# Performance work log

Measured on AMD Instinct MI355X. Metric: run time of the kernel, lower is better.

The kernel has to match this reference:

```python
import jax, jax.numpy as jnp
import numpy as np

P, G, C = 128, 1024, 512
NUM_IDS = 64
EPS_BN = 1e-5


def setup_inputs() -> dict:
    key = jax.random.key(0)
    ks = jax.random.split(key, 20)
    d = jax.random.normal(ks[0], (P, G, C), dtype=jnp.float32)
    y_p = jax.random.randint(ks[1], (P,), 0, NUM_IDS)
    y_g = jax.random.randint(ks[2], (G,), 0, NUM_IDS)
    s = (2.0 / C) ** 0.5  # kaiming-ish scale
    W1 = jax.random.normal(ks[3], (C, C), dtype=jnp.float32) * s
    b1 = jnp.zeros((C,), jnp.float32)
    g1 = 1.0 + 0.02 * jax.random.normal(ks[4], (C,), dtype=jnp.float32)
    be1 = jnp.zeros((C,), jnp.float32)
    rm1 = 0.1 * jax.random.normal(ks[5], (C,), dtype=jnp.float32)
    rv1 = jax.random.uniform(ks[6], (C,), jnp.float32, 0.5, 1.5)
    W2 = jax.random.normal(ks[7], (C, C), dtype=jnp.float32) * s
    b2 = jnp.zeros((C,), jnp.float32)
    g2 = 1.0 + 0.02 * jax.random.normal(ks[8], (C,), dtype=jnp.float32)
    be2 = jnp.zeros((C,), jnp.float32)
    rm2 = 0.1 * jax.random.normal(ks[9], (C,), dtype=jnp.float32)
    rv2 = jax.random.uniform(ks[10], (C,), jnp.float32, 0.5, 1.5)
    # Fc_ClassBlock.classifier: Dropout(0.75) [eval -> identity] + Linear(512, 2)
    Wc = 0.001 * jax.random.normal(ks[11], (C, 2), dtype=jnp.float32)
    bc = jnp.zeros((2,), jnp.float32)
    return dict(d=d, y_p=y_p, y_g=y_g, W1=W1, b1=b1, g1=g1, be1=be1, rm1=rm1, rv1=rv1,
                W2=W2, b2=b2, g2=g2, be2=be2, rm2=rm2, rv2=rv2, Wc=Wc, bc=bc)


def _bn(x, g, b, m, v):
    return (x - m) * jax.lax.rsqrt(v + EPS_BN) * g + b


def _lrelu(x):
    return jnp.where(x >= 0, x, 0.1 * x)


def _preprocess_adj(w):
    # adj = w + I; symmetric normalization D^-1/2 adj^T D^-1/2 (literal torch order)
    adj = w + jnp.eye(w.shape[0], dtype=w.dtype)
    d_inv_sqrt = jax.lax.rsqrt(adj.sum(axis=1))  # rowsum >= 1 due to self-loops
    return d_inv_sqrt[:, None] * adj.T * d_inv_sqrt[None, :]


def reference(d, y_p, y_g, W1, b1, g1, be1, rm1, rv1, W2, b2, g2, be2, rm2, rv2, Wc, bc):
    # label[i, j] = (y_p[i] == y_g[j])
    label = (y_p[:, None] == y_g[None, :]).astype(jnp.int64)
    # hard_weight adjacency: w[i, j] = (y_g[i] == y_g[j])
    w = (y_g[:, None] == y_g[None, :]).astype(jnp.float32)
    w = _preprocess_adj(w)  # [G, G]
    # ReFineBlock (eval mode: BN running stats, dropout off); BN per-feature so flatten P*G
    h = d.reshape(-1, C)
    h = _lrelu(_bn(h @ W1 + b1, g1, be1, rm1, rv1))
    h = _lrelu(_bn(h @ W2 + b2, g2, be2, rm2, rv2))
    t = h.reshape(P, G, C)
    # per-channel torch.mm(t[:, :, i], w) fused into one batched contraction
    d_new = jnp.einsum('pgc,gh->phc', t, w)
    # classifier.classifier: Linear(512, 2) (dropout eval -> identity)
    result = d_new.reshape(-1, C) @ Wc + bc  # [P*G, 2]
    return result, label.reshape(-1)
```

## Files before the change

kernel.cpp:

```cpp
#include <hip/hip_runtime.h>
#include <hip/hip_bf16.h>

#define P_DIM 128
#define G_DIM 1024
#define C_DIM 512
#define M_DIM (P_DIM * G_DIM)
#define NUM_IDS 64
#define RESULT_ELEMS (M_DIM * 2)
#define LABEL_ELEMS  (M_DIM)

typedef __bf16 bf16;
typedef __bf16 bf16x8 __attribute__((ext_vector_type(8)));
typedef float f32x4 __attribute__((ext_vector_type(4)));

constexpr int BM = 64;
constexpr int BK = 32;
constexpr int BNC = 128;
constexpr int APITCH = 40;
constexpr int BPITCH = 40;
constexpr int HPITCH = 520;

__global__ void prep_kernel(const float* __restrict__ b1, const float* __restrict__ g1,
                            const float* __restrict__ be1, const float* __restrict__ rm1,
                            const float* __restrict__ rv1,
                            const float* __restrict__ b2, const float* __restrict__ g2,
                            const float* __restrict__ be2, const float* __restrict__ rm2,
                            const float* __restrict__ rv2,
                            const int* __restrict__ y_g,
                            float* __restrict__ alpha1, float* __restrict__ beta1,
                            float* __restrict__ alpha2, float* __restrict__ beta2,
                            float* __restrict__ inv)
{
    __shared__ int cnt[NUM_IDS];
    int tid = threadIdx.x;
    if (tid < NUM_IDS) cnt[tid] = 0;
    __syncthreads();
    if (tid < C_DIM) {
        float s1 = g1[tid] * rsqrtf(rv1[tid] + 1e-5f);
        alpha1[tid] = s1;
        beta1[tid]  = (b1[tid] - rm1[tid]) * s1 + be1[tid];
        float s2 = g2[tid] * rsqrtf(rv2[tid] + 1e-5f);
        alpha2[tid] = s2;
        beta2[tid]  = (b2[tid] - rm2[tid]) * s2 + be2[tid];
    }
    for (int h = tid; h < G_DIM; h += 512) atomicAdd(&cnt[y_g[h]], 1);
    __syncthreads();
    if (tid < NUM_IDS) inv[tid] = 1.0f / (float)(cnt[tid] + 1);
}

__global__ __launch_bounds__(256) void transpose_scale(
    const float* __restrict__ W, const float* __restrict__ s, bf16* __restrict__ WT)
{
    __shared__ float tile[64][65];
    const int k0 = blockIdx.x * 64, n0 = blockIdx.y * 64;
    const int t = threadIdx.x;
    const int c = t & 63, r4 = t >> 6;
#pragma unroll
    for (int it = 0; it < 16; ++it) {
        int k = r4 + it * 4;
        tile[k][c] = W[(size_t)(k0 + k) * C_DIM + n0 + c];
    }
    __syncthreads();
#pragma unroll
    for (int it = 0; it < 16; ++it) {
        int n = r4 + it * 4;
        float sv = s[n0 + n];
        WT[(size_t)(n0 + n) * C_DIM + k0 + c] = (bf16)(tile[c][n] * sv);
    }
}

__global__ __launch_bounds__(256, 2) void fused_gnn(
    const float* __restrict__ d,
    const bf16* __restrict__ W1T, const float* __restrict__ beta1,
    const bf16* __restrict__ W2T, const float* __restrict__ beta2,
    const float* __restrict__ Wc, float* __restrict__ u)
{
    __shared__ union {
        bf16  As[BM][APITCH];
        float ur[BM][2];
    } sA;
    __shared__ bf16 Bs[BNC][BPITCH];
    __shared__ bf16 h1s[BM][HPITCH];

    const int tid = threadIdx.x;
    const int ln  = tid & 63;
    const int wid = tid >> 6;
    const int wm  = wid & 1;
    const int wn  = wid >> 1;
    const int l15 = ln & 15;
    const int lg  = ln >> 4;
    const size_t gm0 = (size_t)blockIdx.x * BM;

    const int ar = tid >> 2;
    const int aq = (tid & 3) * 8;
    const int bn = tid >> 1;
    const int bq = (tid & 1) * 16;

    for (int chunk = 0; chunk < 4; ++chunk) {
        const int n0 = chunk * BNC;
        f32x4 acc[2][4];
#pragma unroll
        for (int fm = 0; fm < 2; ++fm)
#pragma unroll
            for (int fn = 0; fn < 4; ++fn)
                acc[fm][fn] = (f32x4){0.f, 0.f, 0.f, 0.f};

        float4 pa0 = *(const float4*)(d + (gm0 + ar) * C_DIM + aq);
        float4 pa1 = *(const float4*)(d + (gm0 + ar) * C_DIM + aq + 4);
        float4 pb0 = *(const float4*)(W1T + (size_t)(n0 + bn) * C_DIM + bq);
        float4 pb1 = *(const float4*)(W1T + (size_t)(n0 + bn) * C_DIM + bq + 8);

        for (int k0 = 0; k0 < C_DIM; k0 += BK) {
            __syncthreads();
            {
                bf16x8 av;
                av[0]=(bf16)pa0.x; av[1]=(bf16)pa0.y; av[2]=(bf16)pa0.z; av[3]=(bf16)pa0.w;
                av[4]=(bf16)pa1.x; av[5]=(bf16)pa1.y; av[6]=(bf16)pa1.z; av[7]=(bf16)pa1.w;
                *(bf16x8*)&sA.As[ar][aq] = av;
                *(float4*)&Bs[bn][bq]     = pb0;
                *(float4*)&Bs[bn][bq + 8] = pb1;
            }
            __syncthreads();
            if (k0 + BK < C_DIM) {
                pa0 = *(const float4*)(d + (gm0 + ar) * C_DIM + (k0 + BK) + aq);
                pa1 = *(const float4*)(d + (gm0 + ar) * C_DIM + (k0 + BK) + aq + 4);
                pb0 = *(const float4*)(W1T + (size_t)(n0 + bn) * C_DIM + (k0 + BK) + bq);
                pb1 = *(const float4*)(W1T + (size_t)(n0 + bn) * C_DIM + (k0 + BK) + bq + 8);
            }
            bf16x8 af[2], bfr[4];
#pragma unroll
            for (int fm = 0; fm < 2; ++fm)
                af[fm] = *(const bf16x8*)&sA.As[wm * 32 + fm * 16 + l15][lg * 8];
#pragma unroll
            for (int fn = 0; fn < 4; ++fn)
                bfr[fn] = *(const bf16x8*)&Bs[wn * 64 + fn * 16 + l15][lg * 8];
#pragma unroll
            for (int fm = 0; fm < 2; ++fm)
#pragma unroll
                for (int fn = 0; fn < 4; ++fn)
                    acc[fm][fn] = __builtin_amdgcn_mfma_f32_16x16x32_bf16(
                        af[fm], bfr[fn], acc[fm][fn], 0, 0, 0);
        }
#pragma unroll
        for (int fn = 0; fn < 4; ++fn) {
            int c = n0 + wn * 64 + fn * 16 + l15;
            float be = beta1[c];
#pragma unroll
            for (int fm = 0; fm < 2; ++fm) {
                int mrow = wm * 32 + fm * 16 + lg * 4;
#pragma unroll
                for (int j = 0; j < 4; ++j) {
                    float v = acc[fm][fn][j] + be;
                    v = v >= 0.f ? v : 0.1f * v;
                    h1s[mrow + j][c] = (bf16)v;
                }
            }
        }
    }

    __syncthreads();
    if (tid < BM * 2) sA.ur[tid >> 1][tid & 1] = 0.f;

    float pu0[2][4] = {}, pu1[2][4] = {};
    for (int chunk = 0; chunk < 4; ++chunk) {
        const int n0 = chunk * BNC;
        f32x4 acc[2][4];
#pragma unroll
        for (int fm = 0; fm < 2; ++fm)
#pragma unroll
            for (int fn = 0; fn < 4; ++fn)
                acc[fm][fn] = (f32x4){0.f, 0.f, 0.f, 0.f};

        float4 pb0 = *(const float4*)(W2T + (size_t)(n0 + bn) * C_DIM + bq);
        float4 pb1 = *(const float4*)(W2T + (size_t)(n0 + bn) * C_DIM + bq + 8);

        for (int k0 = 0; k0 < C_DIM; k0 += BK) {
            __syncthreads();
            *(float4*)&Bs[bn][bq]     = pb0;
            *(float4*)&Bs[bn][bq + 8] = pb1;
            __syncthreads();
            if (k0 + BK < C_DIM) {
                pb0 = *(const float4*)(W2T + (size_t)(n0 + bn) * C_DIM + (k0 + BK) + bq);
                pb1 = *(const float4*)(W2T + (size_t)(n0 + bn) * C_DIM + (k0 + BK) + bq + 8);
            }
            bf16x8 af[2], bfr[4];
#pragma unroll
            for (int fm = 0; fm < 2; ++fm)
                af[fm] = *(const bf16x8*)&h1s[wm * 32 + fm * 16 + l15][k0 + lg * 8];
#pragma unroll
            for (int fn = 0; fn < 4; ++fn)
                bfr[fn] = *(const bf16x8*)&Bs[wn * 64 + fn * 16 + l15][lg * 8];
#pragma unroll
            for (int fm = 0; fm < 2; ++fm)
#pragma unroll
                for (int fn = 0; fn < 4; ++fn)
                    acc[fm][fn] = __builtin_amdgcn_mfma_f32_16x16x32_bf16(
                        af[fm], bfr[fn], acc[fm][fn], 0, 0, 0);
        }
#pragma unroll
        for (int fn = 0; fn < 4; ++fn) {
            int c = n0 + wn * 64 + fn * 16 + l15;
            float be = beta2[c];
            float w0 = Wc[2 * c], w1 = Wc[2 * c + 1];
#pragma unroll
            for (int fm = 0; fm < 2; ++fm)
#pragma unroll
                for (int j = 0; j < 4; ++j) {
                    float v = acc[fm][fn][j] + be;
                    v = v >= 0.f ? v : 0.1f * v;
                    pu0[fm][j] = fmaf(v, w0, pu0[fm][j]);
                    pu1[fm][j] = fmaf(v, w1, pu1[fm][j]);
                }
        }
    }
#pragma unroll
    for (int s = 1; s < 16; s <<= 1)
#pragma unroll
        for (int fm = 0; fm < 2; ++fm)
#pragma unroll
            for (int j = 0; j < 4; ++j) {
                pu0[fm][j] += __shfl_xor(pu0[fm][j], s, 64);
                pu1[fm][j] += __shfl_xor(pu1[fm][j], s, 64);
            }
    if (l15 == 0) {
#pragma unroll
        for (int fm = 0; fm < 2; ++fm)
#pragma unroll
            for (int j = 0; j < 4; ++j) {
                int mrow = wm * 32 + fm * 16 + lg * 4 + j;
                atomicAdd(&sA.ur[mrow][0], pu0[fm][j]);
                atomicAdd(&sA.ur[mrow][1], pu1[fm][j]);
            }
    }
    __syncthreads();
    if (tid < BM * 2) {
        int r = tid >> 1, comp = tid & 1;
        u[(gm0 + r) * 2 + comp] = sA.ur[r][comp];
    }
}

__global__ void finalize_kernel(const float* __restrict__ u, const int* __restrict__ y_g,
                                const float* __restrict__ inv, const float* __restrict__ bc,
                                float* __restrict__ out)
{
    int p = blockIdx.x;
    int tid = threadIdx.x;
    __shared__ float su[NUM_IDS][2];
    if (tid < NUM_IDS * 2) su[tid >> 1][tid & 1] = 0.f;
    __syncthreads();
    for (int h = tid; h < G_DIM; h += 256) {
        int k = y_g[h];
        const float* up = u + ((size_t)p * G_DIM + h) * 2;
        atomicAdd(&su[k][0], up[0]);
        atomicAdd(&su[k][1], up[1]);
    }
    __syncthreads();
    float bc0 = bc[0], bc1 = bc[1];
    for (int h = tid; h < G_DIM; h += 256) {
        int k = y_g[h];
        float iv = inv[k];
        size_t r = (size_t)p * G_DIM + h;
        out[r * 2 + 0] = (su[k][0] + u[r * 2 + 0]) * iv + bc0;
        out[r * 2 + 1] = (su[k][1] + u[r * 2 + 1]) * iv + bc1;
    }
}

__global__ void label_kernel(const int* __restrict__ y_p, const int* __restrict__ y_g,
                             float* __restrict__ outF, long long* __restrict__ outL, int mode)
{
    int i = blockIdx.x * 256 + threadIdx.x;
    if (i >= LABEL_ELEMS) return;
    int p = i >> 10;
    int g = i & 1023;
    long long lab = (y_p[p] == y_g[g]) ? 1 : 0;
    if (mode == 1) outF[i] = (float)lab;
    else           outL[i] = lab;
}

extern "C" void kernel_launch(void* const* d_in, const int* in_sizes, int n_in,
                              void* d_out, int out_size, void* d_ws, size_t ws_size,
                              hipStream_t stream) {
    const float* d   = (const float*)d_in[0];
    const int*   y_p = (const int*)d_in[1];
    const int*   y_g = (const int*)d_in[2];
    const float* W1  = (const float*)d_in[3];
    const float* b1  = (const float*)d_in[4];
    const float* g1  = (const float*)d_in[5];
    const float* be1 = (const float*)d_in[6];
    const float* rm1 = (const float*)d_in[7];
    const float* rv1 = (const float*)d_in[8];
    const float* W2  = (const float*)d_in[9];
    const float* b2  = (const float*)d_in[10];
    const float* g2  = (const float*)d_in[11];
    const float* be2 = (const float*)d_in[12];
    const float* rm2 = (const float*)d_in[13];
    const float* rv2 = (const float*)d_in[14];
    const float* Wc  = (const float*)d_in[15];
    const float* bc  = (const float*)d_in[16];

    float* ws     = (float*)d_ws;
    float* u      = ws;
    float* alpha1 = u + RESULT_ELEMS;
    float* beta1  = alpha1 + C_DIM;
    float* alpha2 = beta1 + C_DIM;
    float* beta2  = alpha2 + C_DIM;
    float* inv    = beta2 + C_DIM;
    bf16*  W1T    = (bf16*)(inv + NUM_IDS);
    bf16*  W2T    = W1T + C_DIM * C_DIM;

    prep_kernel<<<1, 512, 0, stream>>>(b1, g1, be1, rm1, rv1, b2, g2, be2, rm2, rv2,
                                       y_g, alpha1, beta1, alpha2, beta2, inv);

    dim3 tgrid(C_DIM / 64, C_DIM / 64);
    transpose_scale<<<tgrid, 256, 0, stream>>>(W1, alpha1, W1T);
    transpose_scale<<<tgrid, 256, 0, stream>>>(W2, alpha2, W2T);

    fused_gnn<<<M_DIM / BM, 256, 0, stream>>>(d, W1T, beta1, W2T, beta2, Wc, u);

    float* outF = (float*)d_out;
    finalize_kernel<<<P_DIM, 256, 0, stream>>>(u, y_g, inv, bc, outF);

    int mode = 0;
    if (out_size >= RESULT_ELEMS + 2 * LABEL_ELEMS) mode = 2;
    else if (out_size >= RESULT_ELEMS + LABEL_ELEMS) mode = 1;
    if (mode)
        label_kernel<<<(LABEL_ELEMS + 255) / 256, 256, 0, stream>>>(
            y_p, y_g, outF + RESULT_ELEMS, (long long*)(outF + RESULT_ELEMS), mode);
}
```

Before: 731.3 us.

## Split fused GNN into bf16 pre-conversion and two LDS-direct tiled GEMM kernels

The single fused kernel, which kept the first-layer activations in shared memory, is replaced by a separate fp32-to-bf16 conversion of d and two 128x128x64 GEMM kernels. These load tiles directly into LDS with global_load_lds, use an XOR swizzle and a remapped block order. The first GEMM writes bf16 activations to global memory. The second reduces against the classifier weights with global atomics into the output buffer. Weight prep, the label kernel and finalize are merged, and the BN scale is computed inline. This trades large extra global traffic (bf16 copies of d and of h1, each 128 MB) for bigger tiles, higher MMA density and asynchronous loads.

```diff
diff --git a/kernel.cpp b/kernel.cpp
--- a/kernel.cpp
+++ b/kernel.cpp
@@ -13,12 +13,11 @@
 typedef __bf16 bf16x8 __attribute__((ext_vector_type(8)));
 typedef float f32x4 __attribute__((ext_vector_type(4)));
 
-constexpr int BM = 64;
-constexpr int BK = 32;
-constexpr int BNC = 128;
-constexpr int APITCH = 40;
-constexpr int BPITCH = 40;
-constexpr int HPITCH = 520;
+__device__ __forceinline__ void gload_lds16(const bf16* g, bf16* l) {
+    __builtin_amdgcn_global_load_lds(
+        (const __attribute__((address_space(1))) void*)g,
+        (__attribute__((address_space(3))) void*)l, 16, 0, 0);
+}
 
 __global__ void prep_kernel(const float* __restrict__ b1, const float* __restrict__ g1,
                             const float* __restrict__ be1, const float* __restrict__ rm1,
@@ -27,8 +26,7 @@
                             const float* __restrict__ be2, const float* __restrict__ rm2,
                             const float* __restrict__ rv2,
                             const int* __restrict__ y_g,
-                            float* __restrict__ alpha1, float* __restrict__ beta1,
-                            float* __restrict__ alpha2, float* __restrict__ beta2,
+                            float* __restrict__ beta1, float* __restrict__ beta2,
                             float* __restrict__ inv)
 {
     __shared__ int cnt[NUM_IDS];
@@ -37,20 +35,26 @@
     __syncthreads();
     if (tid < C_DIM) {
         float s1 = g1[tid] * rsqrtf(rv1[tid] + 1e-5f);
-        alpha1[tid] = s1;
-        beta1[tid]  = (b1[tid] - rm1[tid]) * s1 + be1[tid];
+        beta1[tid] = (b1[tid] - rm1[tid]) * s1 + be1[tid];
         float s2 = g2[tid] * rsqrtf(rv2[tid] + 1e-5f);
-        alpha2[tid] = s2;
-        beta2[tid]  = (b2[tid] - rm2[tid]) * s2 + be2[tid];
+        beta2[tid] = (b2[tid] - rm2[tid]) * s2 + be2[tid];
     }
     for (int h = tid; h < G_DIM; h += 512) atomicAdd(&cnt[y_g[h]], 1);
     __syncthreads();
     if (tid < NUM_IDS) inv[tid] = 1.0f / (float)(cnt[tid] + 1);
 }
 
-__global__ __launch_bounds__(256) void transpose_scale(
-    const float* __restrict__ W, const float* __restrict__ s, bf16* __restrict__ WT)
-{
+__global__ __launch_bounds__(256) void wprep(
+    const float* __restrict__ W1, const float* __restrict__ g1, const float* __restrict__ rv1,
+    bf16* __restrict__ W1T,
+    const float* __restrict__ W2, const float* __restrict__ g2, const float* __restrict__ rv2,
+    bf16* __restrict__ W2T)
+{
+    const float* W = blockIdx.z ? W2 : W1;
+    const float* g = blockIdx.z ? g2 : g1;
+    const float* rv = blockIdx.z ? rv2 : rv1;
+    bf16* WT = blockIdx.z ? W2T : W1T;
+
     __shared__ float tile[64][65];
     const int k0 = blockIdx.x * 64, n0 = blockIdx.y * 64;
     const int t = threadIdx.x;
@@ -64,146 +68,121 @@
 #pragma unroll
     for (int it = 0; it < 16; ++it) {
         int n = r4 + it * 4;
-        float sv = s[n0 + n];
+        float sv = g[n0 + n] * rsqrtf(rv[n0 + n] + 1e-5f);
         WT[(size_t)(n0 + n) * C_DIM + k0 + c] = (bf16)(tile[c][n] * sv);
     }
 }
 
-__global__ __launch_bounds__(256, 2) void fused_gnn(
-    const float* __restrict__ d,
-    const bf16* __restrict__ W1T, const float* __restrict__ beta1,
-    const bf16* __restrict__ W2T, const float* __restrict__ beta2,
-    const float* __restrict__ Wc, float* __restrict__ u)
-{
-    __shared__ union {
-        bf16  As[BM][APITCH];
-        float ur[BM][2];
-    } sA;
-    __shared__ bf16 Bs[BNC][BPITCH];
-    __shared__ bf16 h1s[BM][HPITCH];
+__global__ __launch_bounds__(256) void convert_bf16(const float* __restrict__ x,
+                                                    bf16* __restrict__ y)
+{
+    size_t i = ((size_t)blockIdx.x * 256 + threadIdx.x) * 16;
+    float4 a = *(const float4*)(x + i);
+    float4 b = *(const float4*)(x + i + 4);
+    float4 c = *(const float4*)(x + i + 8);
+    float4 e = *(const float4*)(x + i + 12);
+    bf16x8 v0, v1;
+    v0[0]=(bf16)a.x; v0[1]=(bf16)a.y; v0[2]=(bf16)a.z; v0[3]=(bf16)a.w;
+    v0[4]=(bf16)b.x; v0[5]=(bf16)b.y; v0[6]=(bf16)b.z; v0[7]=(bf16)b.w;
+    v1[0]=(bf16)c.x; v1[1]=(bf16)c.y; v1[2]=(bf16)c.z; v1[3]=(bf16)c.w;
+    v1[4]=(bf16)e.x; v1[5]=(bf16)e.y; v1[6]=(bf16)e.z; v1[7]=(bf16)e.w;
+    *(bf16x8*)(y + i) = v0;
+    *(bf16x8*)(y + i + 8) = v1;
+}
+
+template <int MODE>
+__global__ __launch_bounds__(256, 4) void gemm_bt(
+    const bf16* __restrict__ A, const bf16* __restrict__ B,
+    const float* __restrict__ beta, const float* __restrict__ Wc,
+    bf16* __restrict__ Cout, float* __restrict__ u)
+{
+    __shared__ bf16 As[128 * 64];
+    __shared__ bf16 Bs[128 * 64];
+
+    const int orig = blockIdx.x;
+    const int wg = (orig & 7) * 512 + (orig >> 3);
+    const int bx = wg & 3;
+    const int by = wg >> 2;
+    const size_t m0 = (size_t)by * 128;
+    const int n0 = bx * 128;
 
     const int tid = threadIdx.x;
     const int ln  = tid & 63;
-    const int wid = tid >> 6;
-    const int wm  = wid & 1;
-    const int wn  = wid >> 1;
+    const int w   = tid >> 6;
+    const int wm  = w & 1;
+    const int wn  = w >> 1;
     const int l15 = ln & 15;
     const int lg  = ln >> 4;
-    const size_t gm0 = (size_t)blockIdx.x * BM;
-
-    const int ar = tid >> 2;
-    const int aq = (tid & 3) * 8;
-    const int bn = tid >> 1;
-    const int bq = (tid & 1) * 16;
-
-    for (int chunk = 0; chunk < 4; ++chunk) {
-        const int n0 = chunk * BNC;
-        f32x4 acc[2][4];
-#pragma unroll
-        for (int fm = 0; fm < 2; ++fm)
-#pragma unroll
-            for (int fn = 0; fn < 4; ++fn)
-                acc[fm][fn] = (f32x4){0.f, 0.f, 0.f, 0.f};
-
-        float4 pa0 = *(const float4*)(d + (gm0 + ar) * C_DIM + aq);
-        float4 pa1 = *(const float4*)(d + (gm0 + ar) * C_DIM + aq + 4);
-        float4 pb0 = *(const float4*)(W1T + (size_t)(n0 + bn) * C_DIM + bq);
-        float4 pb1 = *(const float4*)(W1T + (size_t)(n0 + bn) * C_DIM + bq + 8);
-
-        for (int k0 = 0; k0 < C_DIM; k0 += BK) {
-            __syncthreads();
-            {
-                bf16x8 av;
-                av[0]=(bf16)pa0.x; av[1]=(bf16)pa0.y; av[2]=(bf16)pa0.z; av[3]=(bf16)pa0.w;
-                av[4]=(bf16)pa1.x; av[5]=(bf16)pa1.y; av[6]=(bf16)pa1.z; av[7]=(bf16)pa1.w;
-                *(bf16x8*)&sA.As[ar][aq] = av;
-                *(float4*)&Bs[bn][bq]     = pb0;
-                *(float4*)&Bs[bn][bq + 8] = pb1;
+
+    const int srow = ln >> 3;
+    const int sw   = (ln & 7) ^ srow;
+    const bf16* Ab = A + (m0 + srow) * C_DIM + sw * 8;
+    const bf16* Bb = B + (size_t)(n0 + srow) * C_DIM + sw * 8;
+
+    f32x4 acc[4][4];
+#pragma unroll
+    for (int i = 0; i < 4; ++i)
+#pragma unroll
+        for (int j = 0; j < 4; ++j) acc[i][j] = (f32x4){0.f, 0.f, 0.f, 0.f};
+
+    for (int k0 = 0; k0 < C_DIM; k0 += 64) {
+        __syncthreads();
+#pragma unroll
+        for (int i = 0; i < 4; ++i) {
+            int c = w * 4 + i;
+            gload_lds16(Ab + (size_t)c * 8 * C_DIM + k0, &As[c * 512]);
+            gload_lds16(Bb + (size_t)c * 8 * C_DIM + k0, &Bs[c * 512]);
+        }
+        __syncthreads();
+#pragma unroll
+        for (int ks = 0; ks < 2; ++ks) {
+            bf16x8 af[4], bfr[4];
+#pragma unroll
+            for (int fm = 0; fm < 4; ++fm) {
+                int row = wm * 64 + fm * 16 + l15;
+                int slot = (ks * 4 + lg) ^ (l15 & 7);
+                af[fm] = *(const bf16x8*)&As[row * 64 + slot * 8];
             }
-            __syncthreads();
-            if (k0 + BK < C_DIM) {
-                pa0 = *(const float4*)(d + (gm0 + ar) * C_DIM + (k0 + BK) + aq);
-                pa1 = *(const float4*)(d + (gm0 + ar) * C_DIM + (k0 + BK) + aq + 4);
-                pb0 = *(const float4*)(W1T + (size_t)(n0 + bn) * C_DIM + (k0 + BK) + bq);
-                pb1 = *(const float4*)(W1T + (size_t)(n0 + bn) * C_DIM + (k0 + BK) + bq + 8);
+#pragma unroll
+            for (int fn = 0; fn < 4; ++fn) {
+                int row = wn * 64 + fn * 16 + l15;
+                int slot = (ks * 4 + lg) ^ (l15 & 7);
+                bfr[fn] = *(const bf16x8*)&Bs[row * 64 + slot * 8];
             }
-            bf16x8 af[2], bfr[4];
-#pragma unroll
-            for (int fm = 0; fm < 2; ++fm)
-                af[fm] = *(const bf16x8*)&sA.As[wm * 32 + fm * 16 + l15][lg * 8];
-#pragma unroll
-            for (int fn = 0; fn < 4; ++fn)
-                bfr[fn] = *(const bf16x8*)&Bs[wn * 64 + fn * 16 + l15][lg * 8];
-#pragma unroll
-            for (int fm = 0; fm < 2; ++fm)
+#pragma unroll
+            for (int fm = 0; fm < 4; ++fm)
 #pragma unroll
                 for (int fn = 0; fn < 4; ++fn)
                     acc[fm][fn] = __builtin_amdgcn_mfma_f32_16x16x32_bf16(
                         af[fm], bfr[fn], acc[fm][fn], 0, 0, 0);
         }
+    }
+
+    if (MODE == 1) {
 #pragma unroll
         for (int fn = 0; fn < 4; ++fn) {
             int c = n0 + wn * 64 + fn * 16 + l15;
-            float be = beta1[c];
-#pragma unroll
-            for (int fm = 0; fm < 2; ++fm) {
-                int mrow = wm * 32 + fm * 16 + lg * 4;
+            float be = beta[c];
+#pragma unroll
+            for (int fm = 0; fm < 4; ++fm) {
+                size_t row = m0 + wm * 64 + fm * 16 + lg * 4;
 #pragma unroll
                 for (int j = 0; j < 4; ++j) {
                     float v = acc[fm][fn][j] + be;
                     v = v >= 0.f ? v : 0.1f * v;
-                    h1s[mrow + j][c] = (bf16)v;
+                    Cout[(row + j) * C_DIM + c] = (bf16)v;
                 }
             }
         }
-    }
-
-    __syncthreads();
-    if (tid < BM * 2) sA.ur[tid >> 1][tid & 1] = 0.f;
-
-    float pu0[2][4] = {}, pu1[2][4] = {};
-    for (int chunk = 0; chunk < 4; ++chunk) {
-        const int n0 = chunk * BNC;
-        f32x4 acc[2][4];
-#pragma unroll
-        for (int fm = 0; fm < 2; ++fm)
-#pragma unroll
-            for (int fn = 0; fn < 4; ++fn)
-                acc[fm][fn] = (f32x4){0.f, 0.f, 0.f, 0.f};
-
-        float4 pb0 = *(const float4*)(W2T + (size_t)(n0 + bn) * C_DIM + bq);
-        float4 pb1 = *(const float4*)(W2T + (size_t)(n0 + bn) * C_DIM + bq + 8);
-
-        for (int k0 = 0; k0 < C_DIM; k0 += BK) {
-            __syncthreads();
-            *(float4*)&Bs[bn][bq]     = pb0;
-            *(float4*)&Bs[bn][bq + 8] = pb1;
-            __syncthreads();
-            if (k0 + BK < C_DIM) {
-                pb0 = *(const float4*)(W2T + (size_t)(n0 + bn) * C_DIM + (k0 + BK) + bq);
-                pb1 = *(const float4*)(W2T + (size_t)(n0 + bn) * C_DIM + (k0 + BK) + bq + 8);
-            }
-            bf16x8 af[2], bfr[4];
-#pragma unroll
-            for (int fm = 0; fm < 2; ++fm)
-                af[fm] = *(const bf16x8*)&h1s[wm * 32 + fm * 16 + l15][k0 + lg * 8];
-#pragma unroll
-            for (int fn = 0; fn < 4; ++fn)
-                bfr[fn] = *(const bf16x8*)&Bs[wn * 64 + fn * 16 + l15][lg * 8];
-#pragma unroll
-            for (int fm = 0; fm < 2; ++fm)
-#pragma unroll
-                for (int fn = 0; fn < 4; ++fn)
-                    acc[fm][fn] = __builtin_amdgcn_mfma_f32_16x16x32_bf16(
-                        af[fm], bfr[fn], acc[fm][fn], 0, 0, 0);
-        }
+    } else {
+        float pu0[4][4] = {}, pu1[4][4] = {};
 #pragma unroll
         for (int fn = 0; fn < 4; ++fn) {
             int c = n0 + wn * 64 + fn * 16 + l15;
-            float be = beta2[c];
+            float be = beta[c];
             float w0 = Wc[2 * c], w1 = Wc[2 * c + 1];
 #pragma unroll
-            for (int fm = 0; fm < 2; ++fm)
+            for (int fm = 0; fm < 4; ++fm)
 #pragma unroll
                 for (int j = 0; j < 4; ++j) {
                     float v = acc[fm][fn][j] + be;
@@ -212,36 +191,32 @@
                     pu1[fm][j] = fmaf(v, w1, pu1[fm][j]);
                 }
         }
-    }
-#pragma unroll
-    for (int s = 1; s < 16; s <<= 1)
-#pragma unroll
-        for (int fm = 0; fm < 2; ++fm)
-#pragma unroll
-            for (int j = 0; j < 4; ++j) {
-                pu0[fm][j] += __shfl_xor(pu0[fm][j], s, 64);
-                pu1[fm][j] += __shfl_xor(pu1[fm][j], s, 64);
-            }
-    if (l15 == 0) {
-#pragma unroll
-        for (int fm = 0; fm < 2; ++fm)
-#pragma unroll
-            for (int j = 0; j < 4; ++j) {
-                int mrow = wm * 32 + fm * 16 + lg * 4 + j;
-                atomicAdd(&sA.ur[mrow][0], pu0[fm][j]);
-                atomicAdd(&sA.ur[mrow][1], pu1[fm][j]);
-            }
-    }
-    __syncthreads();
-    if (tid < BM * 2) {
-        int r = tid >> 1, comp = tid & 1;
-        u[(gm0 + r) * 2 + comp] = sA.ur[r][comp];
-    }
-}
-
-__global__ void finalize_kernel(const float* __restrict__ u, const int* __restrict__ y_g,
+#pragma unroll
+        for (int s = 1; s < 16; s <<= 1)
+#pragma unroll
+            for (int fm = 0; fm < 4; ++fm)
+#pragma unroll
+                for (int j = 0; j < 4; ++j) {
+                    pu0[fm][j] += __shfl_xor(pu0[fm][j], s, 64);
+                    pu1[fm][j] += __shfl_xor(pu1[fm][j], s, 64);
+                }
+        if (l15 == 0) {
+#pragma unroll
+            for (int fm = 0; fm < 4; ++fm)
+#pragma unroll
+                for (int j = 0; j < 4; ++j) {
+                    size_t row = m0 + wm * 64 + fm * 16 + lg * 4 + j;
+                    atomicAdd(&u[row * 2 + 0], pu0[fm][j]);
+                    atomicAdd(&u[row * 2 + 1], pu1[fm][j]);
+                }
+        }
+    }
+}
+
+__global__ void finalize_kernel(const float* __restrict__ u, const int* __restrict__ y_p,
+                                const int* __restrict__ y_g,
                                 const float* __restrict__ inv, const float* __restrict__ bc,
-                                float* __restrict__ out)
+                                float* __restrict__ out, int mode)
 {
     int p = blockIdx.x;
     int tid = threadIdx.x;
@@ -256,25 +231,19 @@
     }
     __syncthreads();
     float bc0 = bc[0], bc1 = bc[1];
+    int yp = y_p[p];
+    float* outF2 = out + RESULT_ELEMS;
+    long long* outL = (long long*)(out + RESULT_ELEMS);
     for (int h = tid; h < G_DIM; h += 256) {
         int k = y_g[h];
         float iv = inv[k];
         size_t r = (size_t)p * G_DIM + h;
-        out[r * 2 + 0] = (su[k][0] + u[r * 2 + 0]) * iv + bc0;
-        out[r * 2 + 1] = (su[k][1] + u[r * 2 + 1]) * iv + bc1;
-    }
-}
-
-__global__ void label_kernel(const int* __restrict__ y_p, const int* __restrict__ y_g,
-                             float* __restrict__ outF, long long* __restrict__ outL, int mode)
-{
-    int i = blockIdx.x * 256 + threadIdx.x;
-    if (i >= LABEL_ELEMS) return;
-    int p = i >> 10;
-    int g = i & 1023;
-    long long lab = (y_p[p] == y_g[g]) ? 1 : 0;
-    if (mode == 1) outF[i] = (float)lab;
-    else           outL[i] = lab;
+        float u0 = u[r * 2 + 0], u1 = u[r * 2 + 1];
+        out[r * 2 + 0] = (su[k][0] + u0) * iv + bc0;
+        out[r * 2 + 1] = (su[k][1] + u1) * iv + bc1;
+        if (mode == 2)      outL[r]  = (y_g[h] == yp) ? 1 : 0;
+        else if (mode == 1) outF2[r] = (y_g[h] == yp) ? 1.f : 0.f;
+    }
 }
 
 extern "C" void kernel_launch(void* const* d_in, const int* in_sizes, int n_in,
@@ -298,32 +267,33 @@
     const float* Wc  = (const float*)d_in[15];
     const float* bc  = (const float*)d_in[16];
 
-    float* ws     = (float*)d_ws;
-    float* u      = ws;
-    float* alpha1 = u + RESULT_ELEMS;
-    float* beta1  = alpha1 + C_DIM;
-    float* alpha2 = beta1 + C_DIM;
-    float* beta2  = alpha2 + C_DIM;
-    float* inv    = beta2 + C_DIM;
-    bf16*  W1T    = (bf16*)(inv + NUM_IDS);
-    bf16*  W2T    = W1T + C_DIM * C_DIM;
+    float* ws    = (float*)d_ws;
+    float* beta1 = ws;
+    float* beta2 = beta1 + C_DIM;
+    float* inv   = beta2 + C_DIM;
+    bf16*  dbf   = (bf16*)(inv + NUM_IDS);
+    bf16*  h1    = dbf + (size_t)M_DIM * C_DIM;
+    bf16*  W1T   = h1 + (size_t)M_DIM * C_DIM;
+    bf16*  W2T   = W1T + C_DIM * C_DIM;
+
+    float* outF = (float*)d_out;
+    float* u    = outF;
+
+    hipMemsetAsync(u, 0, RESULT_ELEMS * sizeof(float), stream);
 
     prep_kernel<<<1, 512, 0, stream>>>(b1, g1, be1, rm1, rv1, b2, g2, be2, rm2, rv2,
-                                       y_g, alpha1, beta1, alpha2, beta2, inv);
-
-    dim3 tgrid(C_DIM / 64, C_DIM / 64);
-    transpose_scale<<<tgrid, 256, 0, stream>>>(W1, alpha1, W1T);
-    transpose_scale<<<tgrid, 256, 0, stream>>>(W2, alpha2, W2T);
-
-    fused_gnn<<<M_DIM / BM, 256, 0, stream>>>(d, W1T, beta1, W2T, beta2, Wc, u);
-
-    float* outF = (float*)d_out;
-    finalize_kernel<<<P_DIM, 256, 0, stream>>>(u, y_g, inv, bc, outF);
+                                       y_g, beta1, beta2, inv);
+
+    dim3 tgrid(C_DIM / 64, C_DIM / 64, 2);
+    wprep<<<tgrid, 256, 0, stream>>>(W1, g1, rv1, W1T, W2, g2, rv2, W2T);
+
+    convert_bf16<<<M_DIM * C_DIM / (256 * 16), 256, 0, stream>>>(d, dbf);
+
+    gemm_bt<1><<<4096, 256, 0, stream>>>(dbf, W1T, beta1, nullptr, h1, nullptr);
+    gemm_bt<2><<<4096, 256, 0, stream>>>(h1, W2T, beta2, Wc, nullptr, u);
 
     int mode = 0;
     if (out_size >= RESULT_ELEMS + 2 * LABEL_ELEMS) mode = 2;
     else if (out_size >= RESULT_ELEMS + LABEL_ELEMS) mode = 1;
-    if (mode)
-        label_kernel<<<(LABEL_ELEMS + 255) / 256, 256, 0, stream>>>(
-            y_p, y_g, outF + RESULT_ELEMS, (long long*)(outF + RESULT_ELEMS), mode);
-}
+    finalize_kernel<<<P_DIM, 256, 0, stream>>>(u, y_p, y_g, inv, bc, outF, mode);
+}
```

After: 662.5 us. 1.1x faster.
